# Kernel tuning notes

Hardware: AMD Instinct MI355X
Metric: run time of the kernel (lower is better)

Reference implementation:

```python
import jax, jax.numpy as jnp
import numpy as np

GROUPS = 16
EPS_GN = 1e-6
EPS_L2 = 1e-12


def setup_inputs() -> dict:
    key = jax.random.key(0)
    ks = jax.random.split(key, 5)
    B, C, H, W = 8, 256, 64, 64
    s = 0.02
    return {
        "x": jax.random.normal(ks[0], (B, C, H, W), dtype=jnp.float32),
        "gn_gamma": jnp.ones((C,), dtype=jnp.float32),
        "gn_beta": jnp.zeros((C,), dtype=jnp.float32),
        "qkv_w": jax.random.normal(ks[1], (3 * C, C), dtype=jnp.float32) * s,
        "qkv_b": jax.random.normal(ks[2], (3 * C,), dtype=jnp.float32) * s,
        "temperature": jnp.ones((1, 1, 1), dtype=jnp.float32),  # (num_heads,1,1)
        "proj_w": jax.random.normal(ks[3], (C, C), dtype=jnp.float32) * s,
        "proj_b": jax.random.normal(ks[4], (C,), dtype=jnp.float32) * s,
    }


def _group_norm(x, gamma, beta):
    B, C, H, W = x.shape
    xg = x.reshape(B, GROUPS, C // GROUPS, H, W)
    mu = xg.mean(axis=(2, 3, 4), keepdims=True)
    var = xg.var(axis=(2, 3, 4), keepdims=True)
    xn = ((xg - mu) * jax.lax.rsqrt(var + EPS_GN)).reshape(B, C, H, W)
    return xn * gamma[None, :, None, None] + beta[None, :, None, None]


def _l2norm(t):
    # normalize along last axis (token axis N), matching F.normalize eps semantics
    n = jnp.sqrt(jnp.sum(t * t, axis=-1, keepdims=True))
    return t / jnp.maximum(n, EPS_L2)


def reference(x, gn_gamma, gn_beta, qkv_w, qkv_b, temperature, proj_w, proj_b):
    B, C, H, W = x.shape
    N = H * W
    nh = 1
    dh = C // nh

    h = _group_norm(x, gn_gamma, gn_beta).reshape(B, C, N).transpose(0, 2, 1)  # (B,N,C)

    qkv = h @ qkv_w.T + qkv_b                                   # (B,N,3C)
    qkv = qkv.reshape(B, N, 3, nh, dh).transpose(2, 0, 3, 4, 1)  # (3,B,nh,dh,N)
    q, k, v = qkv[0], qkv[1], qkv[2]

    q = _l2norm(q)
    k = _l2norm(k)

    # channel cross-covariance attention: (B,nh,dh,dh)
    attn = jax.nn.softmax(jnp.einsum('bhcn,bhdn->bhcd', q, k) * temperature[None], axis=-1)
    out = jnp.einsum('bhcd,bhdn->bhcn', attn, v)                 # (B,nh,dh,N)
    out = out.transpose(0, 3, 1, 2).reshape(B, N, C)             # (B,N,C)
    out = out @ proj_w.T + proj_b

    return x + out.transpose(0, 2, 1).reshape(B, C, H, W)
```

## Files before the change

### kernel.cpp

```cpp
#include <hip/hip_runtime.h>
#include <hip/hip_bf16.h>

namespace {

constexpr float EPS_GN = 1e-6f;
constexpr float EPS_L2 = 1e-12f;

typedef __attribute__((ext_vector_type(8))) short bf16x8;
typedef __attribute__((ext_vector_type(4))) float f32x4;

__device__ __forceinline__ unsigned short f2bf(float f) {
  union { __hip_bfloat16 h; unsigned short u; } cv;
  cv.h = __float2bfloat16(f);
  return cv.u;
}
__device__ __forceinline__ float blo(unsigned u) { return __uint_as_float(u << 16); }
__device__ __forceinline__ float bhi(unsigned u) { return __uint_as_float(u & 0xffff0000u); }

__global__ __launch_bounds__(256) void cvt_bf_k(const float* __restrict__ src,
                                                unsigned short* __restrict__ dst, int n4) {
  int i = blockIdx.x * 256 + threadIdx.x;
  if (i < n4) {
    float4 v = ((const float4*)src)[i];
    unsigned p0 = f2bf(v.x) | ((unsigned)f2bf(v.y) << 16);
    unsigned p1 = f2bf(v.z) | ((unsigned)f2bf(v.w) << 16);
    ((int2*)dst)[i] = make_int2((int)p0, (int)p1);
  }
}

__global__ __launch_bounds__(256) void cvt_t_k(const float* __restrict__ src,
                                               unsigned short* __restrict__ dst) {
  __shared__ float tl[64][65];
  const int j0 = blockIdx.y * 64, d0 = blockIdx.x * 64;
  const int t = threadIdx.x;
  const int jr = t >> 2, ds = (t & 3) * 16;
#pragma unroll
  for (int q = 0; q < 4; ++q) {
    float4 v = *(const float4*)(src + (size_t)(j0 + jr) * 256 + d0 + ds + q * 4);
    tl[jr][ds + q * 4 + 0] = v.x; tl[jr][ds + q * 4 + 1] = v.y;
    tl[jr][ds + q * 4 + 2] = v.z; tl[jr][ds + q * 4 + 3] = v.w;
  }
  __syncthreads();
  const int dr = t >> 2, js = (t & 3) * 16;
  unsigned pk[8];
#pragma unroll
  for (int q = 0; q < 8; ++q)
    pk[q] = f2bf(tl[js + 2 * q][dr]) | ((unsigned)f2bf(tl[js + 2 * q + 1][dr]) << 16);
  int4 o1 = make_int4((int)pk[0], (int)pk[1], (int)pk[2], (int)pk[3]);
  int4 o2 = make_int4((int)pk[4], (int)pk[5], (int)pk[6], (int)pk[7]);
  unsigned short* dp = dst + (size_t)(d0 + dr) * 256 + j0 + js;
  *(int4*)dp = o1;
  *(int4*)(dp + 8) = o2;
}

__global__ __launch_bounds__(256) void xprep_k(const float* __restrict__ x,
                                               unsigned short* __restrict__ xbf,
                                               unsigned short* __restrict__ xT,
                                               float* __restrict__ sxpart) {
  __shared__ unsigned short tl[64][68];
  const int b = blockIdx.z, c0 = blockIdx.y * 64, n0 = blockIdx.x * 64;
  const int t = threadIdx.x;
  const int cl = t >> 2, ns = (t & 3) * 16;
  const float* xp = x + ((size_t)b << 20) + (size_t)(c0 + cl) * 4096 + n0 + ns;
  unsigned pk[8];
  float s = 0.f;
#pragma unroll
  for (int q = 0; q < 4; ++q) {
    float4 v = *(const float4*)(xp + q * 4);
    s += v.x + v.y + v.z + v.w;
    pk[2 * q + 0] = f2bf(v.x) | ((unsigned)f2bf(v.y) << 16);
    pk[2 * q + 1] = f2bf(v.z) | ((unsigned)f2bf(v.w) << 16);
  }
  unsigned short* xo = xbf + ((size_t)b << 20) + (size_t)(c0 + cl) * 4096 + n0 + ns;
  *(int4*)xo = make_int4((int)pk[0], (int)pk[1], (int)pk[2], (int)pk[3]);
  *(int4*)(xo + 8) = make_int4((int)pk[4], (int)pk[5], (int)pk[6], (int)pk[7]);
#pragma unroll
  for (int q = 0; q < 8; ++q)
    *(unsigned*)(&tl[cl][ns + 2 * q]) = pk[q];
  s += __shfl_xor(s, 1);
  s += __shfl_xor(s, 2);
  if ((t & 3) == 0)
    sxpart[((size_t)((b * 4 + blockIdx.y) * 64 + cl)) * 64 + blockIdx.x] = s;
  __syncthreads();
  const int nl = t >> 2, cs2 = (t & 3) * 16;
  unsigned pk2[8];
#pragma unroll
  for (int q = 0; q < 8; ++q)
    pk2[q] = (unsigned)(unsigned short)tl[cs2 + 2 * q][nl] |
             ((unsigned)(unsigned short)tl[cs2 + 2 * q + 1][nl] << 16);
  unsigned short* to = xT + ((size_t)((b << 12) + n0 + nl)) * 256 + c0 + cs2;
  *(int4*)to = make_int4((int)pk2[0], (int)pk2[1], (int)pk2[2], (int)pk2[3]);
  *(int4*)(to + 8) = make_int4((int)pk2[4], (int)pk2[5], (int)pk2[6], (int)pk2[7]);
}

struct NTArgs {
  const unsigned short* A; long abst; int lda;
  const unsigned short* B; long bbst; int ldb;
  int K; int zdiv;
  float* outF; long ostF; int ldc;
  unsigned short* outU; long ostU;
  const float* qs; const float* wsv; const float* qkvb; const float* temp;
  const float* hvec; const float* xres;
};
enum { EPI_F32 = 0, EPI_BF16 = 1, EPI_LOGITS = 2, EPI_OUT = 3 };

template <int EPI>
__global__ __launch_bounds__(256) void nt64_k(NTArgs p) {
  __shared__ unsigned short As[4096];
  __shared__ unsigned short Bs[4096];
  const int z = blockIdx.z;
  const int b = z / p.zdiv, sl = z % p.zdiv;
  const int kper = p.K / p.zdiv;
  const int m0 = blockIdx.y * 64, n0 = blockIdx.x * 64;
  const int tid = threadIdx.x;
  const int l = tid & 63, w = tid >> 6;
  const int wm = w >> 1, wn = w & 1;

  const int r = tid >> 2;
  const unsigned short* aG = p.A + (size_t)b * p.abst + (size_t)(m0 + r) * p.lda +
                             (size_t)sl * kper + (tid & 3) * 16;
  const unsigned short* bG = p.B + (size_t)b * p.bbst + (size_t)(n0 + r) * p.ldb +
                             (size_t)sl * kper + (tid & 3) * 16;
  const int g0 = (tid & 3) * 2;
  const int w0 = r * 128 + (((g0)     ^ (r & 7)) << 4);
  const int w1 = r * 128 + (((g0 + 1) ^ (r & 7)) << 4);

  int rdA[2], rdB[2];
#pragma unroll
  for (int i = 0; i < 2; ++i) {
    int rm = wm * 32 + i * 16 + (l & 15);
    rdA[i] = rm * 128 + (((l >> 4) ^ (rm & 7)) << 4);
    int rn = wn * 32 + i * 16 + (l & 15);
    rdB[i] = rn * 128 + (((l >> 4) ^ (rn & 7)) << 4);
  }

  f32x4 zero = {0.f, 0.f, 0.f, 0.f};
  f32x4 acc[2][2] = {{zero, zero}, {zero, zero}};

  const int ksteps = kper >> 6;
  for (int ks = 0; ks < ksteps; ++ks) {
    int4 a0 = *(const int4*)aG, a1 = *(const int4*)(aG + 8);
    int4 b0 = *(const int4*)bG, b1 = *(const int4*)(bG + 8);
    aG += 64; bG += 64;
    __syncthreads();
    *(int4*)((char*)As + w0) = a0; *(int4*)((char*)As + w1) = a1;
    *(int4*)((char*)Bs + w0) = b0; *(int4*)((char*)Bs + w1) = b1;
    __syncthreads();
#pragma unroll
    for (int kk = 0; kk < 2; ++kk) {
      bf16x8 af[2], bf_[2];
#pragma unroll
      for (int i = 0; i < 2; ++i) {
        af[i]  = *(const bf16x8*)((const char*)As + (rdA[i] ^ (kk << 6)));
        bf_[i] = *(const bf16x8*)((const char*)Bs + (rdB[i] ^ (kk << 6)));
      }
#pragma unroll
      for (int i = 0; i < 2; ++i)
#pragma unroll
        for (int j = 0; j < 2; ++j)
          acc[i][j] = __builtin_amdgcn_mfma_f32_16x16x32_bf16(af[i], bf_[j], acc[i][j], 0, 0, 0);
    }
  }

  const int ml = wm * 32 + ((l >> 4) << 2);
  const int nl = wn * 32 + (l & 15);
  const int mB = m0 + ml, nB = n0 + nl;

  if (EPI == EPI_F32) {
    float* po = p.outF + (size_t)z * p.ostF;
#pragma unroll
    for (int i = 0; i < 2; ++i)
#pragma unroll
      for (int rr = 0; rr < 4; ++rr)
#pragma unroll
        for (int j = 0; j < 2; ++j)
          po[(size_t)(mB + i * 16 + rr) * p.ldc + nB + j * 16] = acc[i][j][rr];
  } else if (EPI == EPI_BF16) {
    unsigned short* pu = p.outU + (size_t)z * p.ostU;
#pragma unroll
    for (int i = 0; i < 2; ++i)
#pragma unroll
      for (int rr = 0; rr < 4; ++rr)
#pragma unroll
        for (int j = 0; j < 2; ++j)
          pu[(size_t)(mB + i * 16 + rr) * p.ldc + nB + j * 16] = f2bf(acc[i][j][rr]);
  } else if (EPI == EPI_LOGITS) {
    const float T = p.temp[0];
#pragma unroll
    for (int i = 0; i < 2; ++i) {
#pragma unroll
      for (int rr = 0; rr < 4; ++rr) {
        int mi = mB + i * 16 + rr;
        float qsv = p.qs[z * 512 + mi];
        float bq = p.qkvb[mi];
        float wqsv = p.wsv[z * 512 + mi];
#pragma unroll
        for (int j = 0; j < 2; ++j) {
          int nj = nB + j * 16;
          float ksv = p.qs[z * 512 + 256 + nj];
          float bk = p.qkvb[256 + nj];
          float wksv = p.wsv[z * 512 + 256 + nj];
          float v = acc[i][j][rr] + bq * wksv + bk * wqsv + 4096.f * bq * bk;
          p.outF[(size_t)z * p.ostF + (size_t)mi * p.ldc + nj] = T * qsv * ksv * v;
        }
      }
    }
  } else {
#pragma unroll
    for (int i = 0; i < 2; ++i) {
#pragma unroll
      for (int rr = 0; rr < 4; ++rr) {
        int mi = mB + i * 16 + rr;
        float hv = p.hvec[z * 256 + mi];
        size_t rowo = ((size_t)z << 20) + (size_t)mi * 4096;
#pragma unroll
        for (int j = 0; j < 2; ++j)
          p.outF[rowo + nB + j * 16] =
              acc[i][j][rr] + hv + p.xres[rowo + nB + j * 16];
      }
    }
  }
}

__global__ __launch_bounds__(256) void stats_k(
    const float* __restrict__ part, const float* __restrict__ sxpart,
    const float* __restrict__ gamma, const float* __restrict__ beta,
    const unsigned short* __restrict__ qkvw_bf,
    float* __restrict__ avec, float* __restrict__ evec,
    float* __restrict__ svec, float* __restrict__ sxvec,
    float* __restrict__ wsv) {
  const int b = blockIdx.x, c = threadIdx.x;
  const float* sp = sxpart + ((size_t)(b * 256 + c) << 6);
  float sxv = 0.f;
#pragma unroll 4
  for (int t = 0; t < 64; ++t) sxv += sp[t];
  float dg = 0.f;
#pragma unroll
  for (int s = 0; s < 4; ++s) dg += part[((size_t)(b * 4 + s) << 16) + c * 257];
  float gs = sxv, g2 = dg;
#pragma unroll
  for (int off = 1; off < 16; off <<= 1) {
    gs += __shfl_xor(gs, off);
    g2 += __shfl_xor(g2, off);
  }
  const float inv = 1.f / 65536.f;
  float mu = gs * inv;
  float var = g2 * inv - mu * mu;
  float rstd = rsqrtf(var + EPS_GN);
  float av = gamma[c] * rstd;
  float ev = beta[c] - mu * av;
  float sv = av * sxv + 4096.f * ev;
  avec[b * 256 + c] = av; evec[b * 256 + c] = ev;
  svec[b * 256 + c] = sv; sxvec[b * 256 + c] = sxv;
  __shared__ float sl_[256];
  sl_[c] = sv;
  __syncthreads();
  for (int i = c; i < 512; i += 256) {
    const unsigned short* wr = qkvw_bf + (size_t)i * 256;
    float acc = 0.f;
    for (int d = 0; d < 256; d += 8) {
      int4 v = *(const int4*)(wr + d);
      acc += blo((unsigned)v.x) * sl_[d + 0] + bhi((unsigned)v.x) * sl_[d + 1];
      acc += blo((unsigned)v.y) * sl_[d + 2] + bhi((unsigned)v.y) * sl_[d + 3];
      acc += blo((unsigned)v.z) * sl_[d + 4] + bhi((unsigned)v.z) * sl_[d + 5];
      acc += blo((unsigned)v.w) * sl_[d + 6] + bhi((unsigned)v.w) * sl_[d + 7];
    }
    wsv[b * 512 + i] = acc;
  }
}

__global__ __launch_bounds__(256) void gfill_k(const float* __restrict__ part,
                                               const float* __restrict__ avec,
                                               const float* __restrict__ evec,
                                               const float* __restrict__ sxvec,
                                               unsigned short* __restrict__ Gbf) {
  const int b = blockIdx.y;
  const int r = blockIdx.x * 16 + (threadIdx.x >> 4);
  const int cs = (threadIdx.x & 15) * 16;
  const float ac = avec[b * 256 + r], ec = evec[b * 256 + r], sxc = sxvec[b * 256 + r];
  unsigned pk[8];
#pragma unroll
  for (int q = 0; q < 8; ++q) {
    unsigned lohi[2];
#pragma unroll
    for (int h = 0; h < 2; ++h) {
      int d = cs + 2 * q + h;
      float S = 0.f;
#pragma unroll
      for (int s = 0; s < 4; ++s)
        S += part[((size_t)(b * 4 + s) << 16) + r * 256 + d];
      float ad = avec[b * 256 + d], ed = evec[b * 256 + d], sxd = sxvec[b * 256 + d];
      float gv = ac * ad * S + ac * ed * sxc + ec * ad * sxd + 4096.f * ec * ed;
      lohi[h] = f2bf(gv);
    }
    pk[q] = lohi[0] | (lohi[1] << 16);
  }
  unsigned short* gp = Gbf + ((size_t)b << 16) + (size_t)r * 256 + cs;
  *(int4*)gp = make_int4((int)pk[0], (int)pk[1], (int)pk[2], (int)pk[3]);
  *(int4*)(gp + 8) = make_int4((int)pk[4], (int)pk[5], (int)pk[6], (int)pk[7]);
}

__global__ __launch_bounds__(256) void scales_k(const unsigned short* __restrict__ Ubf,
                                                const unsigned short* __restrict__ qkvw_bf,
                                                const float* __restrict__ qkv_b,
                                                const float* __restrict__ wsv,
                                                float* __restrict__ qsv) {
  const int row = blockIdx.x * 4 + (threadIdx.x >> 6);
  const int b = row >> 9, i = row & 511;
  const int l = threadIdx.x & 63;
  const unsigned short* ur = Ubf + ((size_t)b << 17) + (size_t)i * 256 + l * 4;
  const unsigned short* wr = qkvw_bf + (size_t)i * 256 + l * 4;
  int2 uv = *(const int2*)ur;
  int2 wv = *(const int2*)wr;
  float dot = blo((unsigned)uv.x) * blo((unsigned)wv.x) + bhi((unsigned)uv.x) * bhi((unsigned)wv.x) +
              blo((unsigned)uv.y) * blo((unsigned)wv.y) + bhi((unsigned)uv.y) * bhi((unsigned)wv.y);
#pragma unroll
  for (int off = 1; off < 64; off <<= 1) dot += __shfl_xor(dot, off);
  if (l == 0) {
    float bi = qkv_b[i], wsi = wsv[b * 512 + i];
    float n2 = dot + 2.f * bi * wsi + 4096.f * bi * bi;
    qsv[b * 512 + i] = 1.f / fmaxf(sqrtf(fmaxf(n2, 0.f)), EPS_L2);
  }
}

__global__ __launch_bounds__(256) void softmax_k(const float* __restrict__ logits,
                                                 unsigned short* __restrict__ Abf) {
  const int bc = blockIdx.x;
  const int j = threadIdx.x;
  float v = logits[((size_t)bc << 8) + j];
  float m = v;
#pragma unroll
  for (int off = 32; off; off >>= 1) m = fmaxf(m, __shfl_xor(m, off));
  __shared__ float sm[4], ssum[4];
  int lane = j & 63, wid = j >> 6;
  if (lane == 0) sm[wid] = m;
  __syncthreads();
  m = fmaxf(fmaxf(sm[0], sm[1]), fmaxf(sm[2], sm[3]));
  float e = expf(v - m);
  float s = e;
#pragma unroll
  for (int off = 32; off; off >>= 1) s += __shfl_xor(s, off);
  if (lane == 0) ssum[wid] = s;
  __syncthreads();
  s = ssum[0] + ssum[1] + ssum[2] + ssum[3];
  Abf[((size_t)bc << 8) + j] = f2bf(e / s);
}

__global__ __launch_bounds__(256) void finalize_k(const unsigned short* __restrict__ Abf,
                                                  const float* __restrict__ FT,
                                                  const float* __restrict__ avec,
                                                  const float* __restrict__ evec,
                                                  const float* __restrict__ qkv_b,
                                                  const float* __restrict__ proj_w,
                                                  const float* __restrict__ proj_b,
                                                  unsigned short* __restrict__ Fbf,
                                                  float* __restrict__ hvec) {
  const int b = blockIdx.x, t = threadIdx.x;
  __shared__ float abv[256];
  const unsigned short* ar = Abf + ((size_t)b << 16) + (size_t)t * 256;
  float acc = 0.f;
  for (int j = 0; j < 256; j += 2) {
    unsigned u = *(const unsigned*)(ar + j);
    acc += blo(u) * qkv_b[512 + j] + bhi(u) * qkv_b[512 + j + 1];
  }
  abv[t] = acc;
  __syncthreads();
  float h = proj_b[t];
  const float* pr = proj_w + (size_t)t * 256;
  for (int i = 0; i < 256; ++i) h += pr[i] * abv[i];
  float hc2 = 0.f;
  for (int d = 0; d < 256; ++d) {
    float f = FT[((size_t)b << 16) + (size_t)d * 256 + t];
    hc2 += f * evec[b * 256 + d];
    Fbf[((size_t)b << 16) + (size_t)t * 256 + d] = f2bf(f * avec[b * 256 + d]);
  }
  hvec[b * 256 + t] = h + hc2;
}

}

extern "C" void kernel_launch(void* const* d_in, const int* in_sizes, int n_in,
                              void* d_out, int out_size, void* d_ws, size_t ws_size,
                              hipStream_t stream) {
  const float* x      = (const float*)d_in[0];
  const float* gamma  = (const float*)d_in[1];
  const float* beta   = (const float*)d_in[2];
  const float* qkv_w  = (const float*)d_in[3];
  const float* qkv_b  = (const float*)d_in[4];
  const float* temp   = (const float*)d_in[5];
  const float* proj_w = (const float*)d_in[6];
  const float* proj_b = (const float*)d_in[7];
  float* out = (float*)d_out;

  char* ws = (char*)d_ws;
  const size_t MB = 1048576;
  unsigned short* qkvw_bf = (unsigned short*)(ws);
  unsigned short* pw_bf   = (unsigned short*)(ws + 0x60000);
  unsigned short* wvt_bf  = (unsigned short*)(ws + 0x80000);
  float* avec   = (float*)(ws + 0xA0000);
  float* evec   = (float*)(ws + 0xA2000);
  float* svec   = (float*)(ws + 0xA4000);
  float* sxvec  = (float*)(ws + 0xA6000);
  float* wsv    = (float*)(ws + 0xA8000);
  float* qsv    = (float*)(ws + 0xAC000);
  float* hvec   = (float*)(ws + 0xB0000);
  float* sxpart = (float*)(ws + 1 * MB);
  float* part   = (float*)(ws + 2 * MB);
  unsigned short* Gbf  = (unsigned short*)(ws + 10 * MB);
  unsigned short* Ubf  = (unsigned short*)(ws + 11 * MB);
  float* logits        = (float*)(ws + 13 * MB);
  unsigned short* Abf  = (unsigned short*)(ws + 15 * MB);
  unsigned short* Y1   = (unsigned short*)(ws + 16 * MB);
  float* FT            = (float*)(ws + 17 * MB);
  unsigned short* Fbf  = (unsigned short*)(ws + 19 * MB);
  unsigned short* xbf  = (unsigned short*)(ws + 20 * MB);
  unsigned short* xT   = (unsigned short*)(ws + 36 * MB);
  if (ws_size < 52 * MB) return;

  cvt_bf_k<<<192, 256, 0, stream>>>(qkv_w, qkvw_bf, 768 * 256 / 4);
  cvt_bf_k<<<64, 256, 0, stream>>>(proj_w, pw_bf, 256 * 256 / 4);
  cvt_t_k<<<dim3(4, 4), 256, 0, stream>>>(qkv_w + 512 * 256, wvt_bf);

  xprep_k<<<dim3(64, 4, 8), 256, 0, stream>>>(x, xbf, xT, sxpart);

  {
    NTArgs p{};
    p.A = xbf; p.abst = 1L << 20; p.lda = 4096;
    p.B = xbf; p.bbst = 1L << 20; p.ldb = 4096;
    p.K = 4096; p.zdiv = 4;
    p.outF = part; p.ostF = 65536; p.ldc = 256;
    nt64_k<EPI_F32><<<dim3(4, 4, 32), 256, 0, stream>>>(p);
  }

  stats_k<<<8, 256, 0, stream>>>(part, sxpart, gamma, beta, qkvw_bf,
                                 avec, evec, svec, sxvec, wsv);
  gfill_k<<<dim3(16, 8), 256, 0, stream>>>(part, avec, evec, sxvec, Gbf);

  {
    NTArgs p{};
    p.A = qkvw_bf; p.abst = 0; p.lda = 256;
    p.B = Gbf; p.bbst = 65536; p.ldb = 256;
    p.K = 256; p.zdiv = 1;
    p.outU = Ubf; p.ostU = 131072; p.ldc = 256;
    nt64_k<EPI_BF16><<<dim3(4, 8, 8), 256, 0, stream>>>(p);
  }

  scales_k<<<1024, 256, 0, stream>>>(Ubf, qkvw_bf, qkv_b, wsv, qsv);

  {
    NTArgs p{};
    p.A = Ubf; p.abst = 131072; p.lda = 256;
    p.B = qkvw_bf + 256 * 256; p.bbst = 0; p.ldb = 256;
    p.K = 256; p.zdiv = 1;
    p.outF = logits; p.ostF = 65536; p.ldc = 256;
    p.qs = qsv; p.wsv = wsv; p.qkvb = qkv_b; p.temp = temp;
    nt64_k<EPI_LOGITS><<<dim3(4, 4, 8), 256, 0, stream>>>(p);
  }

  softmax_k<<<2048, 256, 0, stream>>>(logits, Abf);

  {
    NTArgs p{};
    p.A = wvt_bf; p.abst = 0; p.lda = 256;
    p.B = Abf; p.bbst = 65536; p.ldb = 256;
    p.K = 256; p.zdiv = 1;
    p.outU = Y1; p.ostU = 65536; p.ldc = 256;
    nt64_k<EPI_BF16><<<dim3(4, 4, 8), 256, 0, stream>>>(p);
  }

  {
    NTArgs p{};
    p.A = Y1; p.abst = 65536; p.lda = 256;
    p.B = pw_bf; p.bbst = 0; p.ldb = 256;
    p.K = 256; p.zdiv = 1;
    p.outF = FT; p.ostF = 65536; p.ldc = 256;
    nt64_k<EPI_F32><<<dim3(4, 4, 8), 256, 0, stream>>>(p);
  }

  finalize_k<<<8, 256, 0, stream>>>(Abf, FT, avec, evec, qkv_b, proj_w, proj_b,
                                    Fbf, hvec);

  {
    NTArgs p{};
    p.A = Fbf; p.abst = 65536; p.lda = 256;
    p.B = xT; p.bbst = 1L << 20; p.ldb = 256;
    p.K = 256; p.zdiv = 1;
    p.outF = out; p.ostF = 0; p.ldc = 4096;
    p.hvec = hvec; p.xres = x;
    nt64_k<EPI_OUT><<<dim3(64, 4, 8), 256, 0, stream>>>(p);
  }
}
```

Measured before the change: 132.1 us.

## Exploit Gram symmetry and fold residual add into output GEMM via identity

The x·xᵀ Gram GEMM now launches only the 10 upper-triangle 64x64 tiles instead of all 16, selected through constant-memory tile index tables. gfill reads mirrored entries for the lower-triangle positions. The residual add is folded algebraically by adding the identity to the bf16 F matrix, so the final GEMM yields (F+I)·x and no longer reads the fp32 x. This removes about a third of the Gram work and a full fp32 read of x. The cost is that the residual term is now carried at bf16 precision instead of exact fp32.

```diff
diff --git a/kernel.cpp b/kernel.cpp
--- a/kernel.cpp
+++ b/kernel.cpp
@@ -8,6 +8,9 @@
 
 typedef __attribute__((ext_vector_type(8))) short bf16x8;
 typedef __attribute__((ext_vector_type(4))) float f32x4;
+
+__device__ __constant__ int c_ti[10] = {0,0,0,0,1,1,1,2,2,3};
+__device__ __constant__ int c_tj[10] = {0,1,2,3,1,2,3,2,3,3};
 
 __device__ __forceinline__ unsigned short f2bf(float f) {
   union { __hip_bfloat16 h; unsigned short u; } cv;
@@ -96,11 +99,11 @@
 struct NTArgs {
   const unsigned short* A; long abst; int lda;
   const unsigned short* B; long bbst; int ldb;
-  int K; int zdiv;
+  int K; int zdiv; int sym;
   float* outF; long ostF; int ldc;
   unsigned short* outU; long ostU;
   const float* qs; const float* wsv; const float* qkvb; const float* temp;
-  const float* hvec; const float* xres;
+  const float* hvec;
 };
 enum { EPI_F32 = 0, EPI_BF16 = 1, EPI_LOGITS = 2, EPI_OUT = 3 };
 
@@ -111,7 +114,9 @@
   const int z = blockIdx.z;
   const int b = z / p.zdiv, sl = z % p.zdiv;
   const int kper = p.K / p.zdiv;
-  const int m0 = blockIdx.y * 64, n0 = blockIdx.x * 64;
+  int m0, n0;
+  if (p.sym) { m0 = c_ti[blockIdx.x] << 6; n0 = c_tj[blockIdx.x] << 6; }
+  else       { m0 = blockIdx.y << 6;       n0 = blockIdx.x << 6; }
   const int tid = threadIdx.x;
   const int l = tid & 63, w = tid >> 6;
   const int wm = w >> 1, wn = w & 1;
@@ -215,8 +220,7 @@
         size_t rowo = ((size_t)z << 20) + (size_t)mi * 4096;
 #pragma unroll
         for (int j = 0; j < 2; ++j)
-          p.outF[rowo + nB + j * 16] =
-              acc[i][j][rr] + hv + p.xres[rowo + nB + j * 16];
+          p.outF[rowo + nB + j * 16] = acc[i][j][rr] + hv;
       }
     }
   }
@@ -227,8 +231,7 @@
     const float* __restrict__ gamma, const float* __restrict__ beta,
     const unsigned short* __restrict__ qkvw_bf,
     float* __restrict__ avec, float* __restrict__ evec,
-    float* __restrict__ svec, float* __restrict__ sxvec,
-    float* __restrict__ wsv) {
+    float* __restrict__ sxvec, float* __restrict__ wsv) {
   const int b = blockIdx.x, c = threadIdx.x;
   const float* sp = sxpart + ((size_t)(b * 256 + c) << 6);
   float sxv = 0.f;
@@ -251,7 +254,7 @@
   float ev = beta[c] - mu * av;
   float sv = av * sxv + 4096.f * ev;
   avec[b * 256 + c] = av; evec[b * 256 + c] = ev;
-  svec[b * 256 + c] = sv; sxvec[b * 256 + c] = sxv;
+  sxvec[b * 256 + c] = sxv;
   __shared__ float sl_[256];
   sl_[c] = sv;
   __syncthreads();
@@ -285,10 +288,11 @@
 #pragma unroll
     for (int h = 0; h < 2; ++h) {
       int d = cs + 2 * q + h;
+      size_t base = ((r >> 6) > (d >> 6)) ? ((size_t)d * 256 + r) : ((size_t)r * 256 + d);
       float S = 0.f;
 #pragma unroll
       for (int s = 0; s < 4; ++s)
-        S += part[((size_t)(b * 4 + s) << 16) + r * 256 + d];
+        S += part[(((size_t)(b * 4 + s)) << 16) + base];
       float ad = avec[b * 256 + d], ed = evec[b * 256 + d], sxd = sxvec[b * 256 + d];
       float gv = ac * ad * S + ac * ed * sxc + ec * ad * sxd + 4096.f * ec * ed;
       lohi[h] = f2bf(gv);
@@ -372,7 +376,8 @@
   for (int d = 0; d < 256; ++d) {
     float f = FT[((size_t)b << 16) + (size_t)d * 256 + t];
     hc2 += f * evec[b * 256 + d];
-    Fbf[((size_t)b << 16) + (size_t)t * 256 + d] = f2bf(f * avec[b * 256 + d]);
+    float fa = f * avec[b * 256 + d] + (d == t ? 1.f : 0.f);
+    Fbf[((size_t)b << 16) + (size_t)t * 256 + d] = f2bf(fa);
   }
   hvec[b * 256 + t] = h + hc2;
 }
@@ -399,7 +404,6 @@
   unsigned short* wvt_bf  = (unsigned short*)(ws + 0x80000);
   float* avec   = (float*)(ws + 0xA0000);
   float* evec   = (float*)(ws + 0xA2000);
-  float* svec   = (float*)(ws + 0xA4000);
   float* sxvec  = (float*)(ws + 0xA6000);
   float* wsv    = (float*)(ws + 0xA8000);
   float* qsv    = (float*)(ws + 0xAC000);
@@ -427,13 +431,13 @@
     NTArgs p{};
     p.A = xbf; p.abst = 1L << 20; p.lda = 4096;
     p.B = xbf; p.bbst = 1L << 20; p.ldb = 4096;
-    p.K = 4096; p.zdiv = 4;
+    p.K = 4096; p.zdiv = 4; p.sym = 1;
     p.outF = part; p.ostF = 65536; p.ldc = 256;
-    nt64_k<EPI_F32><<<dim3(4, 4, 32), 256, 0, stream>>>(p);
+    nt64_k<EPI_F32><<<dim3(10, 1, 32), 256, 0, stream>>>(p);
   }
 
   stats_k<<<8, 256, 0, stream>>>(part, sxpart, gamma, beta, qkvw_bf,
-                                 avec, evec, svec, sxvec, wsv);
+                                 avec, evec, sxvec, wsv);
   gfill_k<<<dim3(16, 8), 256, 0, stream>>>(part, avec, evec, sxvec, Gbf);
 
   {
@@ -486,7 +490,7 @@
     p.B = xT; p.bbst = 1L << 20; p.ldb = 256;
     p.K = 256; p.zdiv = 1;
     p.outF = out; p.ostF = 0; p.ldc = 4096;
-    p.hvec = hvec; p.xres = x;
+    p.hvec = hvec;
     nt64_k<EPI_OUT><<<dim3(64, 4, 8), 256, 0, stream>>>(p);
   }
 }
```

Result: slower. 136.9 us (+3.6%).
